# Kernel tuning notes

Hardware: AMD Instinct MI355X
Metric: run time of the kernel (lower is better)

The kernel has to match this reference:

```python
import jax, jax.numpy as jnp
import numpy as np
import math

H = 128
NUM_RBF = 32
CUTOFF_UPPER = 4.5
CUTOFF_LOWER = 0.0
N_NODES = 16384
N_EDGES = 65536
EPS = 1e-5


def _layernorm(x, gamma, beta):
    m = x.mean(-1, keepdims=True)
    v = ((x - m) ** 2).mean(-1, keepdims=True)
    return (x - m) / jnp.sqrt(v + EPS) * gamma + beta


def _cosine_cutoff(d):
    # cutoff_lower == 0 branch of CosineCutoff
    return 0.5 * (jnp.cos(d * (math.pi / CUTOFF_UPPER)) + 1.0) * (d < CUTOFF_UPPER).astype(d.dtype)


def _expnorm_rbf(d):
    alpha = 5.0 / (CUTOFF_UPPER - CUTOFF_LOWER)
    start = math.exp(-CUTOFF_UPPER + CUTOFF_LOWER)
    means = jnp.linspace(start, 1.0, NUM_RBF, dtype=d.dtype)
    betas = jnp.full((NUM_RBF,), (2.0 / NUM_RBF * (1.0 - start)) ** -2, dtype=d.dtype)
    de = d[:, None]
    return _cosine_cutoff(de) * jnp.exp(-betas * (jnp.exp(alpha * (-de + CUTOFF_LOWER)) - means) ** 2)


def _skew(v):  # [E,3] -> [E,3,3]
    z = jnp.zeros(v.shape[0], v.dtype)
    return jnp.stack([z, -v[:, 2], v[:, 1], v[:, 2], z, -v[:, 0], -v[:, 1], v[:, 0], z], axis=1).reshape(-1, 3, 3)


def _sym(v):  # traceless symmetric part of outer product, [E,3] -> [E,3,3]
    M = v[:, :, None] * v[:, None, :]
    tr3 = (v * v).sum(-1)[:, None, None] / 3.0
    return M - tr3 * jnp.eye(3, dtype=v.dtype)


def _tensor_norm(T):  # [...,3,3] -> [...]
    return (T ** 2).sum((-2, -1))


def setup_inputs() -> dict:
    key = jax.random.key(0)
    ks = jax.random.split(key, 32)
    s = 0.05
    inp = {
        'z': jax.random.randint(ks[0], (N_NODES,), 0, 128, dtype=jnp.int32),
        'pos': jax.random.normal(ks[1], (N_NODES, 3), jnp.float32) * 3.0,
        'batch': jnp.zeros((N_NODES,), jnp.int32),
        'edge_index': jax.random.randint(ks[2], (2, N_EDGES), 0, N_NODES, dtype=jnp.int64),
        'emb_w': jax.random.normal(ks[3], (128, H), jnp.float32) * s,
        'emb2_w': jax.random.normal(ks[4], (H, 2 * H), jnp.float32) * s,
        'emb2_b': jnp.zeros((H,), jnp.float32),
        'dp1_w': jax.random.normal(ks[5], (H, NUM_RBF), jnp.float32) * s,
        'dp1_b': jnp.zeros((H,), jnp.float32),
        'dp2_w': jax.random.normal(ks[6], (H, NUM_RBF), jnp.float32) * s,
        'dp2_b': jnp.zeros((H,), jnp.float32),
        'dp3_w': jax.random.normal(ks[7], (H, NUM_RBF), jnp.float32) * s,
        'dp3_b': jnp.zeros((H,), jnp.float32),
        'lt0_w': jax.random.normal(ks[8], (H, H), jnp.float32) * s,
        'lt1_w': jax.random.normal(ks[9], (H, H), jnp.float32) * s,
        'lt2_w': jax.random.normal(ks[10], (H, H), jnp.float32) * s,
        'ls0_w': jax.random.normal(ks[11], (2 * H, H), jnp.float32) * s,
        'ls0_b': jnp.zeros((2 * H,), jnp.float32),
        'ls1_w': jax.random.normal(ks[12], (3 * H, 2 * H), jnp.float32) * s,
        'ls1_b': jnp.zeros((3 * H,), jnp.float32),
        'in_gamma': jnp.ones((H,), jnp.float32),
        'in_beta': jnp.zeros((H,), jnp.float32),
        'lin_w': jax.random.normal(ks[13], (H, 3 * H), jnp.float32) * s,
        'lin_b': jnp.zeros((H,), jnp.float32),
        'on_gamma': jnp.ones((3 * H,), jnp.float32),
        'on_beta': jnp.zeros((3 * H,), jnp.float32),
        'ol1_w': jax.random.normal(ks[14], (H // 2, H), jnp.float32) * s,
        'ol1_b': jnp.zeros((H // 2,), jnp.float32),
        'ol2_w': jax.random.normal(ks[15], (1, H // 2), jnp.float32) * s,
        'ol2_b': jnp.zeros((1,), jnp.float32),
    }
    return inp


def reference(z, pos, batch, edge_index, emb_w, emb2_w, emb2_b, dp1_w, dp1_b, dp2_w, dp2_b,
              dp3_w, dp3_b, lt0_w, lt1_w, lt2_w, ls0_w, ls0_b, ls1_w, ls1_b,
              in_gamma, in_beta, lin_w, lin_b, on_gamma, on_beta, ol1_w, ol1_b, ol2_w, ol2_b):
    src, dst = edge_index[0], edge_index[1]
    edge_vec = pos[src] - pos[dst]                            # [E,3]
    edge_weight = jnp.sqrt((edge_vec ** 2).sum(-1))           # [E]
    edge_attr = _expnorm_rbf(edge_weight)                     # [E,R]
    self_mask = src == dst
    edge_vec_norm = edge_vec / jnp.where(self_mask, 1.0, edge_weight)[:, None]

    # atomic-number message: Zij = emb2(concat(emb[z_src], emb[z_dst]))
    Zemb = emb_w[z]                                           # [N,H]
    Zcat = jnp.concatenate([Zemb[src], Zemb[dst]], axis=-1)   # [E,2H]
    Zij = Zcat @ emb2_w.T + emb2_b                            # [E,H]

    C = (_cosine_cutoff(edge_weight)[:, None] * Zij)[:, :, None, None]  # [E,H,1,1]
    eye = jnp.eye(3, dtype=pos.dtype)[None, None]
    d1 = (edge_attr @ dp1_w.T + dp1_b)[:, :, None, None]      # [E,H,1,1]
    d2 = (edge_attr @ dp2_w.T + dp2_b)[:, :, None, None]
    d3 = (edge_attr @ dp3_w.T + dp3_b)[:, :, None, None]
    Iij = d1 * C * eye                                        # [E,H,3,3]
    Aij = d2 * C * _skew(edge_vec_norm)[:, None, :, :]
    Sij = d3 * C * _sym(edge_vec_norm)[:, None, :, :]

    N = pos.shape[0]
    I0 = jax.ops.segment_sum(Iij, src, num_segments=N)        # [N,H,3,3]
    A0 = jax.ops.segment_sum(Aij, src, num_segments=N)
    S0 = jax.ops.segment_sum(Sij, src, num_segments=N)

    tnorm = _layernorm(_tensor_norm(I0 + A0 + S0), in_gamma, in_beta)  # [N,H]
    nrm = jax.nn.silu(tnorm @ ls0_w.T + ls0_b)
    nrm = jax.nn.silu(nrm @ ls1_w.T + ls1_b).reshape(-1, H, 3)          # [N,H,3]

    I = jnp.einsum('nhij,kh->nkij', I0, lt0_w) * nrm[:, :, 0, None, None]
    A = jnp.einsum('nhij,kh->nkij', A0, lt1_w) * nrm[:, :, 1, None, None]
    S = jnp.einsum('nhij,kh->nkij', S0, lt2_w) * nrm[:, :, 2, None, None]

    x = jnp.concatenate([_tensor_norm(I), _tensor_norm(A), _tensor_norm(S)], axis=-1)  # [N,3H]
    x = _layernorm(x, on_gamma, on_beta)
    x = jax.nn.silu(x @ lin_w.T + lin_b)                       # [N,H]
    x = jax.nn.silu(x @ ol1_w.T + ol1_b)                       # [N,H//2]
    y = x @ ol2_w.T + ol2_b                                    # [N,1] per-atom scalar
    return y
```

## Files before the change

kernel.cpp:

```cpp
#include <hip/hip_runtime.h>
#include <math.h>

#define NN 16384
#define NE 65536
#define HH 128

constexpr double D_START = 0.011108996538242306;
constexpr double D_STEP  = (1.0 - D_START) / 31.0;
constexpr float  F_ALPHA = (float)(5.0/4.5);
constexpr double D_BB    = (2.0/32.0)*(1.0 - D_START);
constexpr float  F_BETA  = (float)(1.0/(D_BB*D_BB));
constexpr float  F_PIC   = (float)(M_PI/4.5);

#define POOL_BYTES (16u*1024u*1024u)
__device__ __align__(256) static char g_pool[POOL_BYTES];

typedef __attribute__((ext_vector_type(8))) short bf16x8;
typedef __attribute__((ext_vector_type(4))) float f32x4;

__device__ __forceinline__ float siluf(float x){
  return x * (1.0f/(1.0f + expf(-x)));
}
__device__ __forceinline__ short f2bf(float x){
  unsigned u = __float_as_uint(x);
  unsigned r = (u + 0x7fffu + ((u>>16)&1u)) >> 16;
  return (short)r;
}
__device__ __forceinline__ float bf2f(short h){
  return __uint_as_float(((unsigned)(unsigned short)h)<<16);
}
__device__ __forceinline__ void split_bf(float x, short& h, short& l){
  h = f2bf(x);
  l = f2bf(x - bf2f(h));
}

__global__ __launch_bounds__(256) void k_prep(
    const int* __restrict__ ei, const float* __restrict__ pos,
    const int* __restrict__ z,
    const float* __restrict__ emb_w, const float* __restrict__ emb2_w,
    const float* __restrict__ emb2_b,
    const float* __restrict__ ls0, const float* __restrict__ ls1,
    const float* __restrict__ lin, const float* __restrict__ lt0,
    const float* __restrict__ lt1, const float* __restrict__ lt2,
    const float* __restrict__ dp1, const float* __restrict__ dp2,
    const float* __restrict__ dp3, const float* __restrict__ ol1,
    float* __restrict__ PZ, float* __restrict__ QZ,
    int* __restrict__ bcnt, int* __restrict__ bucket,
    int* __restrict__ ezs, int* __restrict__ ezd, float* __restrict__ ev,
    short* __restrict__ atth, short* __restrict__ attl,
    short* __restrict__ ls0h, short* __restrict__ ls0l,
    short* __restrict__ ls1h, short* __restrict__ ls1l,
    short* __restrict__ linh, short* __restrict__ linl,
    short* __restrict__ lt0h, short* __restrict__ lt0l,
    short* __restrict__ lt1h, short* __restrict__ lt1l,
    short* __restrict__ lt2h, short* __restrict__ lt2l,
    short* __restrict__ dwh, short* __restrict__ dwl,
    short* __restrict__ ol1h, short* __restrict__ ol1l){
  int b = blockIdx.x;
  if (b < 64){
    __shared__ float erow[2][128];
    int sub = threadIdx.x >> 7, h = threadIdx.x & 127;
    int a = b*2 + sub;
    erow[sub][h] = emb_w[a*128 + h];
    __syncthreads();
    float p = 0.f, q = 0.f;
    #pragma unroll 8
    for (int k=0;k<128;++k){
      float e = erow[sub][k];
      p += e * emb2_w[h*256 + k];
      q += e * emb2_w[h*256 + 128 + k];
    }
    PZ[a*128 + h] = p + emb2_b[h];
    QZ[a*128 + h] = q;
    return;
  }
  if (b < 1040){
    int tid = (b-64)*256 + threadIdx.x;
    const float* s; short *dh, *dl; int i;
    if      (tid < 32768)  { s=ls0; dh=ls0h; dl=ls0l; i=tid; }
    else if (tid < 131072) { s=ls1; dh=ls1h; dl=ls1l; i=tid-32768; }
    else if (tid < 180224) { s=lin; dh=linh; dl=linl; i=tid-131072; }
    else if (tid < 196608) { s=lt0; dh=lt0h; dl=lt0l; i=tid-180224; }
    else if (tid < 212992) { s=lt1; dh=lt1h; dl=lt1l; i=tid-196608; }
    else if (tid < 229376) { s=lt2; dh=lt2h; dl=lt2l; i=tid-212992; }
    else if (tid < 241664) {
      int j = tid - 229376;
      int g = j >> 12, idx = j & 4095;
      s = (g==0)?dp1:((g==1)?dp2:dp3);
      short h,l; split_bf(s[idx], h, l);
      dwh[j] = h; dwl[j] = l;
      return;
    }
    else { s=ol1; dh=ol1h; dl=ol1l; i=tid-241664; }
    short h,l; split_bf(s[i], h, l);
    dh[i] = h; dl[i] = l;
    return;
  }
  {
    int e = (b-1040)*256 + threadIdx.x;
    int s = ei[e];
    int t = ei[NE + e];
    float dx = pos[3*s+0] - pos[3*t+0];
    float dy = pos[3*s+1] - pos[3*t+1];
    float dz = pos[3*s+2] - pos[3*t+2];
    float d = sqrtf(dx*dx + dy*dy + dz*dz);
    if (d < 4.5f){
      int g16 = s >> 4;
      int p = atomicAdd(&bcnt[g16], 1);
      if (p < 512) bucket[g16*512 + p] = (e<<4) | (s & 15);
      ezs[e] = z[s];
      ezd[e] = z[t];
      float denom = (s==t) ? 1.0f : d;
      ev[4*e+0] = dx/denom;
      ev[4*e+1] = dy/denom;
      ev[4*e+2] = dz/denom;
      float cut = 0.5f*(cosf(d*F_PIC) + 1.0f);
      ev[4*e+3] = cut;
      float q = expf(-F_ALPHA*d);
      #pragma unroll
      for (int r=0;r<32;++r){
        float m = (float)(D_START + r*D_STEP);
        float u = q - m;
        float a = cut * expf(-F_BETA*u*u);
        short hh, ll; split_bf(a, hh, ll);
        atth[32*e + r] = hh;
        attl[32*e + r] = ll;
      }
    }
  }
}

__global__ __launch_bounds__(512, 4) void k_mega(
    const int* __restrict__ bcnt, const int* __restrict__ bucket,
    const int* __restrict__ ezs, const int* __restrict__ ezd,
    const float* __restrict__ ev,
    const short* __restrict__ atth, const short* __restrict__ attl,
    const short* __restrict__ dwh, const short* __restrict__ dwl,
    const float* __restrict__ db1, const float* __restrict__ db2,
    const float* __restrict__ db3,
    const float* __restrict__ PZ, const float* __restrict__ QZ,
    const float* __restrict__ in_g, const float* __restrict__ in_b,
    const short* __restrict__ w0h, const short* __restrict__ w0l,
    const short* __restrict__ w1h, const short* __restrict__ w1l,
    const short* __restrict__ w2h, const short* __restrict__ w2l,
    const short* __restrict__ ls0h, const short* __restrict__ ls0l,
    const float* __restrict__ ls0b,
    const short* __restrict__ ls1h, const short* __restrict__ ls1l,
    const float* __restrict__ ls1b,
    const short* __restrict__ linh, const short* __restrict__ linl,
    const float* __restrict__ linb,
    const short* __restrict__ ol1h, const short* __restrict__ ol1l,
    const float* __restrict__ ol1b,
    const float* __restrict__ ol2w, const float* __restrict__ ol2b,
    const float* __restrict__ on_g, const float* __restrict__ on_b,
    float* __restrict__ y){
  __shared__ __align__(16) char sm[76288];
  float* Dt    = (float*)sm;
  int*   elocal= (int*)(sm + 24832);
  int*   lcnt  = (int*)(sm + 26880);
  int*   loff  = lcnt + 16;
  int*   lcur  = loff + 17;
  short* T1h   = (short*)sm;
  short* T1l   = (short*)(sm + 9216);
  short* PlnL  = (short*)sm;
  float* xls   = (float*)sm;
  short* X3h   = (short*)sm;
  short* X3l   = (short*)(sm + 5120);
  float* partL = (float*)(sm + 10240);
  int*   tmpb  = (int*)(sm + 51200);
  short* tnhL  = (short*)(sm + 51200);
  short* tnlL  = (short*)(sm + 51200 + 5120);
  float* NRMt  = (float*)(sm + 51200);
  short* xhL   = (short*)(sm + 51200);
  short* xlL   = (short*)(sm + 51200 + 12544);

  int t = threadIdx.x;
  int b = blockIdx.x;
  int w = t >> 6, lane = t & 63;
  int col16 = lane & 15, quad = lane >> 4;
  int bn = b*16;
  int node = t >> 5, q5 = t & 31;

  int ecnt = bcnt[b]; if (ecnt > 512) ecnt = 512;
  if (t < 16){ lcnt[t] = 0; lcur[t] = 0; }
  __syncthreads();
  for (int j = t; j < ecnt; j += 512){
    int val = bucket[b*512 + j];
    tmpb[j] = val;
    atomicAdd(&lcnt[val & 15], 1);
  }
  __syncthreads();
  if (t == 0){
    int a = 0;
    #pragma unroll
    for (int i=0;i<16;++i){ loff[i] = a; a += lcnt[i]; }
    loff[16] = a;
  }
  __syncthreads();
  for (int j = t; j < ecnt; j += 512){
    int val = tmpb[j];
    int nd = val & 15;
    int p = loff[nd] + atomicAdd(&lcur[nd], 1);
    elocal[p] = val >> 4;
  }
  __syncthreads();
  int etot = loff[16];
  int e0n = loff[node], e1n = loff[node+1];

  float pv[10][4];
  #pragma unroll
  for (int p=0;p<10;++p)
    #pragma unroll
    for (int i=0;i<4;++i) pv[p][i]=0.f;

  const float* dbp[3] = {db1, db2, db3};
  for (int c0 = 0; c0 < etot; c0 += 16){
    int jA = c0 + col16; if (jA >= etot) jA = etot - 1;
    int eA = elocal[jA];
    bf16x8 ah = *(const bf16x8*)(atth + (size_t)eA*32 + quad*8);
    bf16x8 al = *(const bf16x8*)(attl + (size_t)eA*32 + quad*8);
    f32x4 dacc[3];
    #pragma unroll
    for (int nt=0;nt<3;++nt) dacc[nt] = (f32x4){0.f,0.f,0.f,0.f};
    #pragma unroll
    for (int nt=0;nt<3;++nt){
      int col = w*48 + nt*16 + col16;
      int g = col >> 7, cg = col & 127;
      bf16x8 wh = *(const bf16x8*)(dwh + g*4096 + cg*32 + quad*8);
      bf16x8 wl = *(const bf16x8*)(dwl + g*4096 + cg*32 + quad*8);
      dacc[nt] = __builtin_amdgcn_mfma_f32_16x16x32_bf16(ah, wh, dacc[nt], 0,0,0);
      dacc[nt] = __builtin_amdgcn_mfma_f32_16x16x32_bf16(ah, wl, dacc[nt], 0,0,0);
      dacc[nt] = __builtin_amdgcn_mfma_f32_16x16x32_bf16(al, wh, dacc[nt], 0,0,0);
    }
    #pragma unroll
    for (int nt=0;nt<3;++nt){
      int col = w*48 + nt*16 + col16;
      int g = col >> 7;
      float bb = dbp[g][col & 127];
      #pragma unroll
      for (int r=0;r<4;++r)
        Dt[(quad*4+r)*388 + col] = dacc[nt][r] + bb;
    }
    __syncthreads();
    int jlo = e0n > c0 ? e0n : c0;
    int jhi0 = c0 + 16; if (jhi0 > etot) jhi0 = etot;
    int jhi = e1n < jhi0 ? e1n : jhi0;
    int h0 = q5*4;
    for (int j = jlo; j < jhi; ++j){
      int le = j - c0;
      int e = elocal[j];
      float4 evv = *(const float4*)(ev + 4*e);
      int zs = ezs[e], zd = ezd[e];
      const float* pz = PZ + zs*128 + h0;
      const float* qz = QZ + zd*128 + h0;
      const float* dr = Dt + le*388 + h0;
      float vx = evv.x, vy = evv.y, vz = evv.z, cut = evv.w;
      float t3v = (vx*vx + vy*vy + vz*vz)*(1.0f/3.0f);
      #pragma unroll
      for (int i=0;i<4;++i){
        float C = cut * (pz[i] + qz[i]);
        float d1 = dr[i], d2 = dr[128+i], d3 = dr[256+i];
        pv[0][i] += d1*C;
        float wa = d2*C;
        pv[1][i] += wa*vx; pv[2][i] += wa*vy; pv[3][i] += wa*vz;
        float ws = d3*C;
        pv[4][i] += ws*(vx*vx - t3v);
        pv[5][i] += ws*(vy*vy - t3v);
        pv[6][i] += ws*(vz*vz - t3v);
        pv[7][i] += ws*(vx*vy);
        pv[8][i] += ws*(vx*vz);
        pv[9][i] += ws*(vy*vz);
      }
    }
    __syncthreads();
  }

  {
    float tnv[4];
    float s8 = 0.f;
    #pragma unroll
    for (int i=0;i<4;++i){
      float x = 3.f*pv[0][i]*pv[0][i]
              + 2.f*(pv[1][i]*pv[1][i]+pv[2][i]*pv[2][i]+pv[3][i]*pv[3][i])
              + (pv[4][i]*pv[4][i]+pv[5][i]*pv[5][i]+pv[6][i]*pv[6][i])
              + 2.f*(pv[7][i]*pv[7][i]+pv[8][i]*pv[8][i]+pv[9][i]*pv[9][i]);
      tnv[i] = x; s8 += x;
    }
    #pragma unroll
    for (int o=16;o;o>>=1) s8 += __shfl_xor(s8, o, 64);
    float mean = s8*(1.0f/128.0f);
    float vq = 0.f;
    #pragma unroll
    for (int i=0;i<4;++i){ float d = tnv[i]-mean; vq += d*d; }
    #pragma unroll
    for (int o=16;o;o>>=1) vq += __shfl_xor(vq, o, 64);
    float rstd = 1.0f/sqrtf(vq*(1.0f/128.0f) + 1e-5f);
    #pragma unroll
    for (int i=0;i<4;++i){
      int h = q5*4 + i;
      float val = (tnv[i]-mean)*rstd*in_g[h] + in_b[h];
      short hh, ll; split_bf(val, hh, ll);
      tnhL[node*160 + h] = hh;
      tnlL[node*160 + h] = ll;
    }
  }
  __syncthreads();

  {
    f32x4 macc[2];
    #pragma unroll
    for (int nt=0;nt<2;++nt) macc[nt] = (f32x4){0.f,0.f,0.f,0.f};
    #pragma unroll
    for (int kc=0; kc<4; ++kc){
      bf16x8 tah = *(const bf16x8*)(tnhL + col16*160 + kc*32 + quad*8);
      bf16x8 tal = *(const bf16x8*)(tnlL + col16*160 + kc*32 + quad*8);
      #pragma unroll
      for (int nt=0;nt<2;++nt){
        int n = w*32 + nt*16 + col16;
        bf16x8 wh = *(const bf16x8*)(ls0h + n*128 + kc*32 + quad*8);
        bf16x8 wl = *(const bf16x8*)(ls0l + n*128 + kc*32 + quad*8);
        macc[nt] = __builtin_amdgcn_mfma_f32_16x16x32_bf16(tah, wh, macc[nt], 0,0,0);
        macc[nt] = __builtin_amdgcn_mfma_f32_16x16x32_bf16(tah, wl, macc[nt], 0,0,0);
        macc[nt] = __builtin_amdgcn_mfma_f32_16x16x32_bf16(tal, wh, macc[nt], 0,0,0);
      }
    }
    #pragma unroll
    for (int nt=0;nt<2;++nt){
      int n = w*32 + nt*16 + col16;
      float bb = ls0b[n];
      #pragma unroll
      for (int r=0;r<4;++r){
        float v = siluf(macc[nt][r] + bb);
        short hh, ll; split_bf(v, hh, ll);
        T1h[(quad*4+r)*288 + n] = hh;
        T1l[(quad*4+r)*288 + n] = ll;
      }
    }
    __syncthreads();
    f32x4 nacc[3];
    #pragma unroll
    for (int nt=0;nt<3;++nt) nacc[nt] = (f32x4){0.f,0.f,0.f,0.f};
    #pragma unroll
    for (int kc=0; kc<8; ++kc){
      bf16x8 tah = *(const bf16x8*)(T1h + col16*288 + kc*32 + quad*8);
      bf16x8 tal = *(const bf16x8*)(T1l + col16*288 + kc*32 + quad*8);
      #pragma unroll
      for (int nt=0;nt<3;++nt){
        int n = w*48 + nt*16 + col16;
        bf16x8 wh = *(const bf16x8*)(ls1h + n*256 + kc*32 + quad*8);
        bf16x8 wl = *(const bf16x8*)(ls1l + n*256 + kc*32 + quad*8);
        nacc[nt] = __builtin_amdgcn_mfma_f32_16x16x32_bf16(tah, wh, nacc[nt], 0,0,0);
        nacc[nt] = __builtin_amdgcn_mfma_f32_16x16x32_bf16(tah, wl, nacc[nt], 0,0,0);
        nacc[nt] = __builtin_amdgcn_mfma_f32_16x16x32_bf16(tal, wh, nacc[nt], 0,0,0);
      }
    }
    __syncthreads();
    #pragma unroll
    for (int nt=0;nt<3;++nt){
      int n = w*48 + nt*16 + col16;
      float bb = ls1b[n];
      #pragma unroll
      for (int r=0;r<4;++r)
        NRMt[(quad*4+r)*388 + n] = siluf(nacc[nt][r] + bb);
    }
  }

  const short* wgh[3] = {w0h, w1h, w2h};
  const short* wgl[3] = {w0l, w1l, w2l};
  float xI[4], xA[4], xS[4];
  #pragma unroll
  for (int r=0;r<4;++r){ xI[r]=0.f; xA[r]=0.f; xS[r]=0.f; }
  #pragma unroll
  for (int pass=0; pass<2; ++pass){
    const int pbase = pass*5;
    __syncthreads();
    #pragma unroll
    for (int pl=0; pl<5; ++pl){
      short* dst = PlnL + (pl*4 + (q5>>3))*1280 + node*80 + ((q5>>1)&3)*16 + (q5&1)*4;
      #pragma unroll
      for (int i=0;i<4;++i){
        short hh, ll; split_bf(pv[pbase+pl][i], hh, ll);
        dst[i] = hh; dst[8+i] = ll;
      }
    }
    __syncthreads();
    f32x4 acc[5];
    #pragma unroll
    for (int pl=0;pl<5;++pl) acc[pl] = (f32x4){0.f,0.f,0.f,0.f};
    #pragma unroll
    for (int hc4=0; hc4<4; ++hc4){
      bf16x8 bh, bl;
      int curg = -1;
      #pragma unroll
      for (int pl=0; pl<5; ++pl){
        const int p = pbase + pl;
        const int g = (p==0)?0:((p<4)?1:2);
        if (g != curg){
          int row = w*16 + col16;
          bh = *(const bf16x8*)(wgh[g] + row*128 + hc4*32 + quad*8);
          bl = *(const bf16x8*)(wgl[g] + row*128 + hc4*32 + quad*8);
          curg = g;
        }
        const short* ab = PlnL + (pl*4 + hc4)*1280 + col16*80 + quad*16;
        bf16x8 ah = *(const bf16x8*)(ab);
        bf16x8 al = *(const bf16x8*)(ab + 8);
        acc[pl] = __builtin_amdgcn_mfma_f32_16x16x32_bf16(ah, bh, acc[pl], 0,0,0);
        acc[pl] = __builtin_amdgcn_mfma_f32_16x16x32_bf16(ah, bl, acc[pl], 0,0,0);
        acc[pl] = __builtin_amdgcn_mfma_f32_16x16x32_bf16(al, bh, acc[pl], 0,0,0);
      }
    }
    #pragma unroll
    for (int pl=0; pl<5; ++pl){
      const int p = pbase + pl;
      const int sel = (p==0)?0:((p<4)?1:2);
      int k = w*16 + col16;
      #pragma unroll
      for (int r=0; r<4; ++r){
        int nloc = quad*4 + r;
        float n = NRMt[nloc*388 + 3*k + sel];
        float v = acc[pl][r]*n;
        if (p==0)      xI[r]  = 3.f*v*v;
        else if (p<4)  xA[r] += 2.f*v*v;
        else if (p<7)  xS[r] += v*v;
        else           xS[r] += 2.f*v*v;
      }
    }
  }
  __syncthreads();

  {
    int k = w*16 + col16;
    #pragma unroll
    for (int r=0; r<4; ++r){
      int nloc = quad*4 + r;
      xls[nloc*388 + k]       = xI[r];
      xls[nloc*388 + 128 + k] = xA[r];
      xls[nloc*388 + 256 + k] = xS[r];
    }
  }
  __syncthreads();
  {
    float vv[12];
    float s = 0.f;
    #pragma unroll
    for (int i=0;i<12;++i){ vv[i] = xls[node*388 + q5*12 + i]; s += vv[i]; }
    #pragma unroll
    for (int o=16;o;o>>=1) s += __shfl_xor(s, o, 64);
    float mean = s*(1.0f/384.0f);
    float qsum = 0.f;
    #pragma unroll
    for (int i=0;i<12;++i){ float d = vv[i]-mean; qsum += d*d; }
    #pragma unroll
    for (int o=16;o;o>>=1) qsum += __shfl_xor(qsum, o, 64);
    float rstd = 1.0f/sqrtf(qsum*(1.0f/384.0f) + 1e-5f);
    #pragma unroll
    for (int i=0;i<12;++i){
      int c = q5*12 + i;
      float val = (vv[i]-mean)*rstd*on_g[c] + on_b[c];
      short hh, ll; split_bf(val, hh, ll);
      xhL[node*392 + c] = hh;
      xlL[node*392 + c] = ll;
    }
  }
  __syncthreads();

  {
    f32x4 lacc = (f32x4){0.f,0.f,0.f,0.f};
    int n = w*16 + col16;
    #pragma unroll
    for (int kc=0; kc<12; ++kc){
      bf16x8 xah = *(const bf16x8*)(xhL + col16*392 + kc*32 + quad*8);
      bf16x8 xal = *(const bf16x8*)(xlL + col16*392 + kc*32 + quad*8);
      bf16x8 wh = *(const bf16x8*)(linh + n*384 + kc*32 + quad*8);
      bf16x8 wl = *(const bf16x8*)(linl + n*384 + kc*32 + quad*8);
      lacc = __builtin_amdgcn_mfma_f32_16x16x32_bf16(xah, wh, lacc, 0,0,0);
      lacc = __builtin_amdgcn_mfma_f32_16x16x32_bf16(xah, wl, lacc, 0,0,0);
      lacc = __builtin_amdgcn_mfma_f32_16x16x32_bf16(xal, wh, lacc, 0,0,0);
    }
    __syncthreads();
    float bb = linb[n];
    #pragma unroll
    for (int r=0;r<4;++r){
      float v = siluf(lacc[r] + bb);
      short hh, ll; split_bf(v, hh, ll);
      X3h[(quad*4+r)*160 + n] = hh;
      X3l[(quad*4+r)*160 + n] = ll;
    }
    __syncthreads();
  }

  if (w < 4){
    f32x4 hacc = (f32x4){0.f,0.f,0.f,0.f};
    int n = w*16 + col16;
    #pragma unroll
    for (int kc=0; kc<4; ++kc){
      bf16x8 xah = *(const bf16x8*)(X3h + col16*160 + kc*32 + quad*8);
      bf16x8 xal = *(const bf16x8*)(X3l + col16*160 + kc*32 + quad*8);
      bf16x8 wh = *(const bf16x8*)(ol1h + n*128 + kc*32 + quad*8);
      bf16x8 wl = *(const bf16x8*)(ol1l + n*128 + kc*32 + quad*8);
      hacc = __builtin_amdgcn_mfma_f32_16x16x32_bf16(xah, wh, hacc, 0,0,0);
      hacc = __builtin_amdgcn_mfma_f32_16x16x32_bf16(xah, wl, hacc, 0,0,0);
      hacc = __builtin_amdgcn_mfma_f32_16x16x32_bf16(xal, wh, hacc, 0,0,0);
    }
    float b1 = ol1b[n], w2 = ol2w[n];
    #pragma unroll
    for (int r=0;r<4;++r){
      float v = siluf(hacc[r] + b1) * w2;
      #pragma unroll
      for (int o=8;o;o>>=1) v += __shfl_xor(v, o, 64);
      if (col16 == 0) partL[w*16 + quad*4 + r] = v;
    }
  }
  __syncthreads();
  if (t < 16)
    y[bn + t] = partL[t] + partL[16+t] + partL[32+t] + partL[48+t] + ol2b[0];
}

extern "C" void kernel_launch(void* const* d_in, const int* in_sizes, int n_in,
                              void* d_out, int out_size, void* d_ws, size_t ws_size,
                              hipStream_t stream) {
  const int*   z      = (const int*)d_in[0];
  const float* pos    = (const float*)d_in[1];
  const int*   ei     = (const int*)d_in[3];
  const float* emb_w  = (const float*)d_in[4];
  const float* emb2_w = (const float*)d_in[5];
  const float* emb2_b = (const float*)d_in[6];
  const float* dp1_w  = (const float*)d_in[7];
  const float* dp1_b  = (const float*)d_in[8];
  const float* dp2_w  = (const float*)d_in[9];
  const float* dp2_b  = (const float*)d_in[10];
  const float* dp3_w  = (const float*)d_in[11];
  const float* dp3_b  = (const float*)d_in[12];
  const float* lt0_w  = (const float*)d_in[13];
  const float* lt1_w  = (const float*)d_in[14];
  const float* lt2_w  = (const float*)d_in[15];
  const float* ls0_w  = (const float*)d_in[16];
  const float* ls0_b  = (const float*)d_in[17];
  const float* ls1_w  = (const float*)d_in[18];
  const float* ls1_b  = (const float*)d_in[19];
  const float* in_g   = (const float*)d_in[20];
  const float* in_b   = (const float*)d_in[21];
  const float* lin_w  = (const float*)d_in[22];
  const float* lin_b  = (const float*)d_in[23];
  const float* on_g   = (const float*)d_in[24];
  const float* on_b   = (const float*)d_in[25];
  const float* ol1_w  = (const float*)d_in[26];
  const float* ol1_b  = (const float*)d_in[27];
  const float* ol2_w  = (const float*)d_in[28];
  const float* ol2_b  = (const float*)d_in[29];
  float* out = (float*)d_out;

  const size_t NEED = 14u*1024u*1024u;
  char* wsb = (char*)d_ws;
  if (ws_size < NEED){
    void* p = nullptr;
    hipGetSymbolAddress(&p, HIP_SYMBOL(g_pool));
    wsb = (char*)p;
  }
  size_t off = 0;
  auto alloc = [&](size_t bytes)->void*{
    void* p = wsb + off;
    off = (off + bytes + 255) & ~(size_t)255;
    return p;
  };
  float* PZ      = (float*)alloc(128*128*4);
  float* QZ      = (float*)alloc(128*128*4);
  int*   bcnt    = (int*)  alloc(1024*4);
  int*   bucket  = (int*)  alloc((size_t)1024*512*4);
  int*   ezs     = (int*)  alloc(NE*4);
  int*   ezd     = (int*)  alloc(NE*4);
  float* ev      = (float*)alloc((size_t)NE*4*4);
  short* atth    = (short*)alloc((size_t)NE*32*2);
  short* attl    = (short*)alloc((size_t)NE*32*2);
  short* dwh     = (short*)alloc(3*128*32*2);
  short* dwl     = (short*)alloc(3*128*32*2);
  short* ls0h    = (short*)alloc(256*128*2);
  short* ls0l    = (short*)alloc(256*128*2);
  short* ls1h    = (short*)alloc(384*256*2);
  short* ls1l    = (short*)alloc(384*256*2);
  short* linh    = (short*)alloc(128*384*2);
  short* linl    = (short*)alloc(128*384*2);
  short* lt0h    = (short*)alloc(128*128*2);
  short* lt0l    = (short*)alloc(128*128*2);
  short* lt1h    = (short*)alloc(128*128*2);
  short* lt1l    = (short*)alloc(128*128*2);
  short* lt2h    = (short*)alloc(128*128*2);
  short* lt2l    = (short*)alloc(128*128*2);
  short* ol1h    = (short*)alloc(64*128*2);
  short* ol1l    = (short*)alloc(64*128*2);

  hipMemsetAsync(bcnt, 0, 1024*4, stream);

  k_prep<<<1296, 256, 0, stream>>>(ei, pos, z, emb_w, emb2_w, emb2_b,
                                   ls0_w, ls1_w, lin_w, lt0_w, lt1_w, lt2_w,
                                   dp1_w, dp2_w, dp3_w, ol1_w,
                                   PZ, QZ, bcnt, bucket, ezs, ezd, ev, atth, attl,
                                   ls0h, ls0l, ls1h, ls1l, linh, linl,
                                   lt0h, lt0l, lt1h, lt1l, lt2h, lt2l,
                                   dwh, dwl, ol1h, ol1l);
  k_mega<<<NN/16, 512, 0, stream>>>(bcnt, bucket, ezs, ezd, ev, atth, attl,
                                    dwh, dwl, dp1_b, dp2_b, dp3_b,
                                    PZ, QZ, in_g, in_b,
                                    lt0h, lt0l, lt1h, lt1l, lt2h, lt2l,
                                    ls0h, ls0l, ls0_b, ls1h, ls1l, ls1_b,
                                    linh, linl, lin_b, ol1h, ol1l, ol1_b,
                                    ol2_w, ol2_b, on_g, on_b, out);
}
```

Baseline: 264.8 us.

## Compute per-edge RBF features inside mega kernel instead of storing to global

Per-edge geometry, cutoff, atom types and RBF expansion (bf16 hi/lo split) are no longer written to global buffers by the prep kernel. The mega kernel now recomputes them per 16-edge chunk into shared memory. This cuts global traffic (about 8 MB of attention features plus the edge arrays) and shrinks shared memory from about 76 KB to about 53 KB, which may allow more resident blocks. In exchange it adds two block-wide barriers per edge chunk, serialized work on 16 threads, and splits the output projection into five smaller passes with extra syncs.

```diff
diff --git a/kernel.cpp b/kernel.cpp
--- a/kernel.cpp
+++ b/kernel.cpp
@@ -12,7 +12,7 @@
 constexpr float  F_BETA  = (float)(1.0/(D_BB*D_BB));
 constexpr float  F_PIC   = (float)(M_PI/4.5);
 
-#define POOL_BYTES (16u*1024u*1024u)
+#define POOL_BYTES (8u*1024u*1024u)
 __device__ __align__(256) static char g_pool[POOL_BYTES];
 
 typedef __attribute__((ext_vector_type(8))) short bf16x8;
@@ -36,7 +36,6 @@
 
 __global__ __launch_bounds__(256) void k_prep(
     const int* __restrict__ ei, const float* __restrict__ pos,
-    const int* __restrict__ z,
     const float* __restrict__ emb_w, const float* __restrict__ emb2_w,
     const float* __restrict__ emb2_b,
     const float* __restrict__ ls0, const float* __restrict__ ls1,
@@ -46,8 +45,6 @@
     const float* __restrict__ dp3, const float* __restrict__ ol1,
     float* __restrict__ PZ, float* __restrict__ QZ,
     int* __restrict__ bcnt, int* __restrict__ bucket,
-    int* __restrict__ ezs, int* __restrict__ ezd, float* __restrict__ ev,
-    short* __restrict__ atth, short* __restrict__ attl,
     short* __restrict__ ls0h, short* __restrict__ ls0l,
     short* __restrict__ ls1h, short* __restrict__ ls1l,
     short* __restrict__ linh, short* __restrict__ linl,
@@ -108,33 +105,14 @@
       int g16 = s >> 4;
       int p = atomicAdd(&bcnt[g16], 1);
       if (p < 512) bucket[g16*512 + p] = (e<<4) | (s & 15);
-      ezs[e] = z[s];
-      ezd[e] = z[t];
-      float denom = (s==t) ? 1.0f : d;
-      ev[4*e+0] = dx/denom;
-      ev[4*e+1] = dy/denom;
-      ev[4*e+2] = dz/denom;
-      float cut = 0.5f*(cosf(d*F_PIC) + 1.0f);
-      ev[4*e+3] = cut;
-      float q = expf(-F_ALPHA*d);
-      #pragma unroll
-      for (int r=0;r<32;++r){
-        float m = (float)(D_START + r*D_STEP);
-        float u = q - m;
-        float a = cut * expf(-F_BETA*u*u);
-        short hh, ll; split_bf(a, hh, ll);
-        atth[32*e + r] = hh;
-        attl[32*e + r] = ll;
-      }
     }
   }
 }
 
 __global__ __launch_bounds__(512, 4) void k_mega(
     const int* __restrict__ bcnt, const int* __restrict__ bucket,
-    const int* __restrict__ ezs, const int* __restrict__ ezd,
-    const float* __restrict__ ev,
-    const short* __restrict__ atth, const short* __restrict__ attl,
+    const int* __restrict__ ei, const float* __restrict__ pos,
+    const int* __restrict__ zA,
     const short* __restrict__ dwh, const short* __restrict__ dwl,
     const float* __restrict__ db1, const float* __restrict__ db2,
     const float* __restrict__ db3,
@@ -154,7 +132,7 @@
     const float* __restrict__ ol2w, const float* __restrict__ ol2b,
     const float* __restrict__ on_g, const float* __restrict__ on_b,
     float* __restrict__ y){
-  __shared__ __align__(16) char sm[76288];
+  __shared__ __align__(16) char sm[53248];
   float* Dt    = (float*)sm;
   int*   elocal= (int*)(sm + 24832);
   int*   lcnt  = (int*)(sm + 26880);
@@ -167,12 +145,19 @@
   short* X3h   = (short*)sm;
   short* X3l   = (short*)(sm + 5120);
   float* partL = (float*)(sm + 10240);
-  int*   tmpb  = (int*)(sm + 51200);
-  short* tnhL  = (short*)(sm + 51200);
-  short* tnlL  = (short*)(sm + 51200 + 5120);
-  float* NRMt  = (float*)(sm + 51200);
-  short* xhL   = (short*)(sm + 51200);
-  short* xlL   = (short*)(sm + 51200 + 12544);
+  char*  Bb    = sm + 28160;
+  int*   tmpb  = (int*)Bb;
+  float4* evL  = (float4*)Bb;
+  float* qL    = (float*)(Bb + 256);
+  int*   zsL   = (int*)(Bb + 320);
+  int*   zdL   = (int*)(Bb + 384);
+  short* attH  = (short*)(Bb + 448);
+  short* attL2 = (short*)(Bb + 1472);
+  short* tnhL  = (short*)Bb;
+  short* tnlL  = (short*)(Bb + 5120);
+  float* NRMt  = (float*)Bb;
+  short* xhL   = (short*)Bb;
+  short* xlL   = (short*)(Bb + 12544);
 
   int t = threadIdx.x;
   int b = blockIdx.x;
@@ -215,10 +200,34 @@
 
   const float* dbp[3] = {db1, db2, db3};
   for (int c0 = 0; c0 < etot; c0 += 16){
-    int jA = c0 + col16; if (jA >= etot) jA = etot - 1;
-    int eA = elocal[jA];
-    bf16x8 ah = *(const bf16x8*)(atth + (size_t)eA*32 + quad*8);
-    bf16x8 al = *(const bf16x8*)(attl + (size_t)eA*32 + quad*8);
+    if (t < 16){
+      int j = c0 + t; if (j >= etot) j = etot - 1;
+      int e = elocal[j];
+      int s = ei[e], tt2 = ei[NE + e];
+      float dx = pos[3*s+0] - pos[3*tt2+0];
+      float dy = pos[3*s+1] - pos[3*tt2+1];
+      float dz = pos[3*s+2] - pos[3*tt2+2];
+      float d = sqrtf(dx*dx + dy*dy + dz*dz);
+      float denom = (s==tt2) ? 1.0f : d;
+      float cut = 0.5f*(cosf(d*F_PIC) + 1.0f);
+      evL[t] = make_float4(dx/denom, dy/denom, dz/denom, cut);
+      qL[t] = expf(-F_ALPHA*d);
+      zsL[t] = zA[s];
+      zdL[t] = zA[tt2];
+    }
+    __syncthreads();
+    {
+      int le = t >> 5, r = t & 31;
+      float m = (float)(D_START + r*D_STEP);
+      float u = qL[le] - m;
+      float a = evL[le].w * expf(-F_BETA*u*u);
+      short hh, ll; split_bf(a, hh, ll);
+      attH[le*32 + r]  = hh;
+      attL2[le*32 + r] = ll;
+    }
+    __syncthreads();
+    bf16x8 ah = *(const bf16x8*)(attH  + col16*32 + quad*8);
+    bf16x8 al = *(const bf16x8*)(attL2 + col16*32 + quad*8);
     f32x4 dacc[3];
     #pragma unroll
     for (int nt=0;nt<3;++nt) dacc[nt] = (f32x4){0.f,0.f,0.f,0.f};
@@ -248,9 +257,8 @@
     int h0 = q5*4;
     for (int j = jlo; j < jhi; ++j){
       int le = j - c0;
-      int e = elocal[j];
-      float4 evv = *(const float4*)(ev + 4*e);
-      int zs = ezs[e], zd = ezd[e];
+      float4 evv = evL[le];
+      int zs = zsL[le], zd = zdL[le];
       const float* pz = PZ + zs*128 + h0;
       const float* qz = QZ + zd*128 + h0;
       const float* dr = Dt + le*388 + h0;
@@ -371,11 +379,11 @@
   #pragma unroll
   for (int r=0;r<4;++r){ xI[r]=0.f; xA[r]=0.f; xS[r]=0.f; }
   #pragma unroll
-  for (int pass=0; pass<2; ++pass){
-    const int pbase = pass*5;
-    __syncthreads();
-    #pragma unroll
-    for (int pl=0; pl<5; ++pl){
+  for (int pass=0; pass<5; ++pass){
+    const int pbase = pass*2;
+    __syncthreads();
+    #pragma unroll
+    for (int pl=0; pl<2; ++pl){
       short* dst = PlnL + (pl*4 + (q5>>3))*1280 + node*80 + ((q5>>1)&3)*16 + (q5&1)*4;
       #pragma unroll
       for (int i=0;i<4;++i){
@@ -384,15 +392,15 @@
       }
     }
     __syncthreads();
-    f32x4 acc[5];
-    #pragma unroll
-    for (int pl=0;pl<5;++pl) acc[pl] = (f32x4){0.f,0.f,0.f,0.f};
+    f32x4 acc[2];
+    #pragma unroll
+    for (int pl=0;pl<2;++pl) acc[pl] = (f32x4){0.f,0.f,0.f,0.f};
     #pragma unroll
     for (int hc4=0; hc4<4; ++hc4){
       bf16x8 bh, bl;
       int curg = -1;
       #pragma unroll
-      for (int pl=0; pl<5; ++pl){
+      for (int pl=0; pl<2; ++pl){
         const int p = pbase + pl;
         const int g = (p==0)?0:((p<4)?1:2);
         if (g != curg){
@@ -410,7 +418,7 @@
       }
     }
     #pragma unroll
-    for (int pl=0; pl<5; ++pl){
+    for (int pl=0; pl<2; ++pl){
       const int p = pbase + pl;
       const int sel = (p==0)?0:((p<4)?1:2);
       int k = w*16 + col16;
@@ -550,7 +558,7 @@
   const float* ol2_b  = (const float*)d_in[29];
   float* out = (float*)d_out;
 
-  const size_t NEED = 14u*1024u*1024u;
+  const size_t NEED = 4u*1024u*1024u;
   char* wsb = (char*)d_ws;
   if (ws_size < NEED){
     void* p = nullptr;
@@ -567,11 +575,6 @@
   float* QZ      = (float*)alloc(128*128*4);
   int*   bcnt    = (int*)  alloc(1024*4);
   int*   bucket  = (int*)  alloc((size_t)1024*512*4);
-  int*   ezs     = (int*)  alloc(NE*4);
-  int*   ezd     = (int*)  alloc(NE*4);
-  float* ev      = (float*)alloc((size_t)NE*4*4);
-  short* atth    = (short*)alloc((size_t)NE*32*2);
-  short* attl    = (short*)alloc((size_t)NE*32*2);
   short* dwh     = (short*)alloc(3*128*32*2);
   short* dwl     = (short*)alloc(3*128*32*2);
   short* ls0h    = (short*)alloc(256*128*2);
@@ -591,14 +594,14 @@
 
   hipMemsetAsync(bcnt, 0, 1024*4, stream);
 
-  k_prep<<<1296, 256, 0, stream>>>(ei, pos, z, emb_w, emb2_w, emb2_b,
+  k_prep<<<1296, 256, 0, stream>>>(ei, pos, emb_w, emb2_w, emb2_b,
                                    ls0_w, ls1_w, lin_w, lt0_w, lt1_w, lt2_w,
                                    dp1_w, dp2_w, dp3_w, ol1_w,
-                                   PZ, QZ, bcnt, bucket, ezs, ezd, ev, atth, attl,
+                                   PZ, QZ, bcnt, bucket,
                                    ls0h, ls0l, ls1h, ls1l, linh, linl,
                                    lt0h, lt0l, lt1h, lt1l, lt2h, lt2l,
                                    dwh, dwl, ol1h, ol1l);
-  k_mega<<<NN/16, 512, 0, stream>>>(bcnt, bucket, ezs, ezd, ev, atth, attl,
+  k_mega<<<NN/16, 512, 0, stream>>>(bcnt, bucket, ei, pos, z,
                                     dwh, dwl, dp1_b, dp2_b, dp3_b,
                                     PZ, QZ, in_g, in_b,
                                     lt0h, lt0l, lt1h, lt1l, lt2h, lt2l,
```

Result: slower. 275.8 us (+4.2%).
